# Kernel optimization log

Hardware: AMD Instinct MI355X
Metric: run time of the kernel (lower is better)

Reference implementation:

```python
import jax, jax.numpy as jnp
from jax import lax
import numpy as np

B, T, C = 32, 1024, 512
K = 3
MAX_DUR = 4            # durations drawn from [0,5) -> max value 4
L_MAX = T * MAX_DUR    # static padded mel length (torch pads to batch max; we pad to static max)
EPS = 1e-5


def conv_ln_block(x, w, b, g, beta):
    # x: [B,T,C]; torch ConvLNBlock: permute -> Conv1d(SAME) -> relu -> permute -> LayerNorm -> dropout(eval=id)
    y = lax.conv_general_dilated(x.transpose(0, 2, 1), w, (1,), 'SAME',
                                 dimension_numbers=('NCH', 'OIH', 'NCH')) + b[None, :, None]
    y = jax.nn.relu(y).transpose(0, 2, 1)  # [B,T,Cout]
    mu = y.mean(-1, keepdims=True)
    var = y.var(-1, keepdims=True)
    return (y - mu) * lax.rsqrt(var + EPS) * g + beta


def regulate(batch, durations, token_lengths):
    # Vectorized equivalent of DurationRegulator.inflate: repeat token t durations[b,t] times,
    # concatenate, pad. Implemented as cumsum + searchsorted gather (single pass, no ragged loops).
    pos = jnp.arange(T)
    valid = pos[None, :] < token_lengths[:, None]          # [B,T]
    d = jnp.where(valid, durations, 0)
    total = d.sum(axis=1)
    # torch: if durs.sum()==0 -> fill with 1
    d = jnp.where((total == 0)[:, None], valid.astype(d.dtype), d)
    total = d.sum(axis=1)                                   # [B]
    cum = jnp.cumsum(d, axis=1)                             # inclusive cumsum [B,T]
    frames = jnp.arange(L_MAX)
    idx = jax.vmap(lambda c: jnp.searchsorted(c, frames, side='right'))(cum)  # [B,L_MAX]
    idx = jnp.clip(idx, 0, T - 1)
    out = jnp.take_along_axis(batch, idx[:, :, None], axis=1)                 # [B,L_MAX,C]
    frame_mask = frames[None, :] < total[:, None]
    out = out * frame_mask[:, :, None].astype(batch.dtype)
    return out, total.astype(jnp.float32)


def setup_inputs() -> dict:
    key = jax.random.key(0)
    ks = jax.random.split(key, 8)
    batch = jax.random.normal(ks[0], (B, T, C), dtype=jnp.float32)
    token_lengths = jax.random.randint(ks[1], (B,), T // 2, T + 1).astype(jnp.int32)
    mask = jnp.arange(T)[None, :] < token_lengths[:, None]
    label_durations = jax.random.randint(ks[2], (B, T), 0, MAX_DUR + 1).astype(jnp.int32)
    s1 = 1.0 / np.sqrt(C * K)
    s2 = 1.0 / np.sqrt(C * K)
    params = {
        'conv1_w': jax.random.uniform(ks[3], (C, C, K), minval=-s1, maxval=s1, dtype=jnp.float32),
        'conv1_b': jnp.zeros((C,), jnp.float32),
        'ln1_g': jnp.ones((C,), jnp.float32), 'ln1_b': jnp.zeros((C,), jnp.float32),
        'conv2_w': jax.random.uniform(ks[4], (C, C, K), minval=-s2, maxval=s2, dtype=jnp.float32),
        'conv2_b': jnp.zeros((C,), jnp.float32),
        'ln2_g': jnp.ones((C,), jnp.float32), 'ln2_b': jnp.zeros((C,), jnp.float32),
        'lin_w': jax.random.uniform(ks[5], (C, 1), minval=-1/np.sqrt(C), maxval=1/np.sqrt(C), dtype=jnp.float32),
        'lin_b': jnp.zeros((1,), jnp.float32),
    }
    return dict(batch=batch, token_lengths=token_lengths, mask=mask,
                label_durations=label_durations, **params)


def reference(batch, token_lengths, mask, label_durations,
              conv1_w, conv1_b, ln1_g, ln1_b,
              conv2_w, conv2_b, ln2_g, ln2_b,
              lin_w, lin_b):
    # VariancePredictor: two ConvLN blocks + Linear(out_channels, 1), masked fill 0
    h = conv_ln_block(batch, conv1_w, conv1_b, ln1_g, ln1_b)
    h = conv_ln_block(h, conv2_w, conv2_b, ln2_g, ln2_b)
    predicted_durations = h @ lin_w + lin_b                      # [B,T,1]
    predicted_durations = jnp.where(mask[:, :, None], predicted_durations, 0.0)
    # label_durations provided -> regulator uses labels (training path), alpha=1
    padded_batch, mel_lengths = regulate(batch, label_durations, token_lengths)
    return padded_batch, mel_lengths, predicted_durations
```

## Files before the change

### kernel.cpp

```cpp
#include <hip/hip_runtime.h>
#include <hip/hip_bf16.h>
#include <stdint.h>


typedef _Float16 f16;
typedef _Float16 f16x8 __attribute__((ext_vector_type(8)));
typedef float f32x4 __attribute__((ext_vector_type(4)));

#define B_    32
#define T_    1024
#define TP_   1026
#define C_    512
#define LMAX_ 4096
#define KDIM  1536
#define NK    48

#define XPAD_OFF   0u
#define H1PAD_OFF  33619968u
#define W1T_OFF    67239936u
#define W2T_OFF    68812800u
#define TOT_OFF    137494528u
#define IDX_OFF    137495040u

#define AS1C(p) ((const __attribute__((address_space(1))) void*)(p))
#define AS3(p)  ((__attribute__((address_space(3))) void*)(p))

__global__ __launch_bounds__(256) void prep_pad(const float* __restrict__ batch,
                                                f16* __restrict__ xpad,
                                                f16* __restrict__ h1pad) {
    int row = blockIdx.x * 4 + (threadIdx.x >> 6);
    int lane = threadIdx.x & 63;
    int b = row / TP_, tt = row % TP_;
    size_t dsto = (size_t)row * C_ + lane * 8;
    if (tt == 0 || tt == TP_ - 1) {
        f16x8 z = {};
        *(f16x8*)(xpad + dsto) = z;
        *(f16x8*)(h1pad + dsto) = z;
    } else {
        const float* src = batch + ((size_t)(b * T_ + tt - 1)) * C_ + lane * 8;
        float4 v0 = ((const float4*)src)[0];
        float4 v1 = ((const float4*)src)[1];
        f16x8 h;
        h[0] = (f16)v0.x; h[1] = (f16)v0.y; h[2] = (f16)v0.z; h[3] = (f16)v0.w;
        h[4] = (f16)v1.x; h[5] = (f16)v1.y; h[6] = (f16)v1.z; h[7] = (f16)v1.w;
        *(f16x8*)(xpad + dsto) = h;
    }
}

__global__ __launch_bounds__(256) void prep_w(const float* __restrict__ w1,
                                              const float* __restrict__ w2,
                                              f16* __restrict__ w1t,
                                              f16* __restrict__ w2t) {
    int o = blockIdx.x;
    const float* w = blockIdx.y ? w2 : w1;
    f16* wt = blockIdx.y ? w2t : w1t;
    for (int j = threadIdx.x; j < KDIM; j += 256) {
        int tap = j >> 9, i = j & 511;
        wt[(size_t)o * KDIM + j] = (f16)w[(size_t)o * KDIM + i * 3 + tap];
    }
}

__global__ __launch_bounds__(1024) void scan_kernel(const int* __restrict__ dur,
                                                    const int* __restrict__ tlen,
                                                    int* __restrict__ idxarr,
                                                    int* __restrict__ total,
                                                    float* __restrict__ mel_out) {
    int b = blockIdx.x, t = threadIdx.x;
    __shared__ int sd[1024];
    __shared__ int sv[1024];
    int L = tlen[b];
    int valid = (t < L) ? 1 : 0;
    int d = valid ? dur[b * T_ + t] : 0;
    sd[t] = d; sv[t] = valid;
    __syncthreads();
    for (int off = 1; off < 1024; off <<= 1) {
        int x = 0, y = 0;
        if (t >= off) { x = sd[t - off]; y = sv[t - off]; }
        __syncthreads();
        sd[t] += x; sv[t] += y;
        __syncthreads();
    }
    int totd = sd[1023];
    int cur  = (totd == 0) ? sv[t] : sd[t];
    int prev = (t == 0) ? 0 : ((totd == 0) ? sv[t - 1] : sd[t - 1]);
    for (int f = prev; f < cur; f++) idxarr[b * LMAX_ + f] = t;
    if (t == 1023) {
        int tt = (totd == 0) ? sv[1023] : totd;
        total[b] = tt;
        mel_out[b] = (float)tt;
    }
}

template<int EPI>
__global__ __launch_bounds__(512, 2) void gemm_fused(const f16* __restrict__ A,
                                                     const f16* __restrict__ Bw,
                                                     const float* __restrict__ bias,
                                                     const float* __restrict__ g,
                                                     const float* __restrict__ be,
                                                     const float* __restrict__ lw,
                                                     const float* __restrict__ lb,
                                                     const int* __restrict__ tlen,
                                                     f16* __restrict__ hpad,
                                                     float* __restrict__ pred) {
    __shared__ f16 lds_[40960];
    f16* const A0 = lds_;
    f16* const A1 = lds_ + 4096;
    f16* const B0 = lds_ + 8192;
    f16* const B1 = lds_ + 24576;
    float* red = (float*)lds_;

    const int tid = threadIdx.x;
    const int lane = tid & 63;
    const int w = tid >> 6;
    const int wm = (w & 1) * 64;
    const int wn = (w >> 1) * 128;
    const int m0 = blockIdx.x * 128;
    const int arow0 = (m0 >> 10) * TP_ + (m0 & 1023);

    f32x4 acc[4][8];
#pragma unroll
    for (int i = 0; i < 4; i++)
#pragma unroll
        for (int j = 0; j < 8; j++) acc[i][j] = (f32x4){0.f, 0.f, 0.f, 0.f};

    const int perm = (lane & 3) ^ ((lane >> 2) & 3) ^ ((lane >> 4) & 3);
    const f16* aB = A + (size_t)(arow0 + w * 16 + (lane >> 2)) * C_ + perm * 8;
    const f16* bB = Bw + (size_t)(w * 16 + (lane >> 2)) * KDIM + perm * 8;

#define STAGE(Ad, Bd, kofs) do {                                              \
        __builtin_amdgcn_global_load_lds(AS1C(aB + (kofs)),                   \
                                         AS3((Ad) + w * 512), 16, 0, 0);      \
        _Pragma("unroll")                                                     \
        for (int j_ = 0; j_ < 4; j_++) {                                      \
            __builtin_amdgcn_global_load_lds(                                 \
                AS1C(bB + (size_t)(128 * j_) * KDIM + (kofs)),                \
                AS3((Bd) + (w + 8 * j_) * 512), 16, 0, 0);                    \
        }                                                                     \
    } while (0)

    STAGE(A0, B0, 0);
    __syncthreads();

    f16 *Ac = A0, *An = A1, *Bc = B0, *Bn = B1;
    for (int t = 0; t < NK; ++t) {
        if (t + 1 < NK) STAGE(An, Bn, (t + 1) * 32);
        const int base = perm * 8;
        f16x8 af[4], bf[8];
#pragma unroll
        for (int mi = 0; mi < 4; mi++)
            af[mi] = *(const f16x8*)&Ac[(wm + mi * 16 + (lane & 15)) * 32 + base];
#pragma unroll
        for (int ni = 0; ni < 8; ni++)
            bf[ni] = *(const f16x8*)&Bc[(wn + ni * 16 + (lane & 15)) * 32 + base];
#pragma unroll
        for (int mi = 0; mi < 4; mi++)
#pragma unroll
            for (int ni = 0; ni < 8; ni++)
                acc[mi][ni] = __builtin_amdgcn_mfma_f32_16x16x32_f16(
                    af[mi], bf[ni], acc[mi][ni], 0, 0, 0);
        __syncthreads();
        f16* tp;
        tp = Ac; Ac = An; An = tp;
        tp = Bc; Bc = Bn; Bn = tp;
    }
#undef STAGE

    const int col = lane & 15;
    const int row4 = (lane >> 4) * 4;
    const int nw = w >> 1;

    float bn[8];
#pragma unroll
    for (int ni = 0; ni < 8; ni++) bn[ni] = bias[wn + ni * 16 + col];
    float s_[4][4], q_[4][4];
#pragma unroll
    for (int mi = 0; mi < 4; mi++)
#pragma unroll
        for (int r = 0; r < 4; r++) { s_[mi][r] = 0.f; q_[mi][r] = 0.f; }
#pragma unroll
    for (int mi = 0; mi < 4; mi++)
#pragma unroll
        for (int ni = 0; ni < 8; ni++)
#pragma unroll
            for (int r = 0; r < 4; r++) {
                float v = acc[mi][ni][r] + bn[ni];
                v = v > 0.f ? v : 0.f;
                acc[mi][ni][r] = v;
                s_[mi][r] += v;
                q_[mi][r] += v * v;
            }
#pragma unroll
    for (int m = 8; m; m >>= 1)
#pragma unroll
        for (int mi = 0; mi < 4; mi++)
#pragma unroll
            for (int r = 0; r < 4; r++) {
                s_[mi][r] += __shfl_xor(s_[mi][r], m, 64);
                q_[mi][r] += __shfl_xor(q_[mi][r], m, 64);
            }
    if (col == 0) {
#pragma unroll
        for (int mi = 0; mi < 4; mi++)
#pragma unroll
            for (int r = 0; r < 4; r++) {
                int row = wm + mi * 16 + row4 + r;
                red[(nw * 128 + row) * 2]     = s_[mi][r];
                red[(nw * 128 + row) * 2 + 1] = q_[mi][r];
            }
    }
    __syncthreads();
    float mu_[4][4], rs_[4][4];
#pragma unroll
    for (int mi = 0; mi < 4; mi++)
#pragma unroll
        for (int r = 0; r < 4; r++) {
            int row = wm + mi * 16 + row4 + r;
            float S = red[row * 2]             + red[(128 + row) * 2]
                    + red[(256 + row) * 2]     + red[(384 + row) * 2];
            float Q = red[row * 2 + 1]         + red[(128 + row) * 2 + 1]
                    + red[(256 + row) * 2 + 1] + red[(384 + row) * 2 + 1];
            float mu = S * (1.f / 512.f);
            float x = Q * (1.f / 512.f) - mu * mu + 1e-5f;
            float rs = rsqrtf(x);
            rs = rs * (1.5f - 0.5f * x * rs * rs);
            mu_[mi][r] = mu; rs_[mi][r] = rs;
        }

    if (EPI == 0) {
        const int bb = m0 >> 10, t0 = m0 & 1023;
        f16* hbase = hpad + ((size_t)(bb * TP_ + t0 + 1)) * C_;
#pragma unroll
        for (int ni = 0; ni < 8; ni++) {
            int n = wn + ni * 16 + col;
            float gv = g[n], ev = be[n];
#pragma unroll
            for (int mi = 0; mi < 4; mi++)
#pragma unroll
                for (int r = 0; r < 4; r++) {
                    int lm = wm + mi * 16 + row4 + r;
                    float v = (acc[mi][ni][r] - mu_[mi][r]) * rs_[mi][r] * gv + ev;
                    hbase[(size_t)lm * C_ + n] = (f16)v;
                }
        }
    } else {
        float p_[4][4];
#pragma unroll
        for (int mi = 0; mi < 4; mi++)
#pragma unroll
            for (int r = 0; r < 4; r++) p_[mi][r] = 0.f;
#pragma unroll
        for (int ni = 0; ni < 8; ni++) {
            int n = wn + ni * 16 + col;
            float gv = g[n], ev = be[n], wv = lw[n];
#pragma unroll
            for (int mi = 0; mi < 4; mi++)
#pragma unroll
                for (int r = 0; r < 4; r++)
                    p_[mi][r] += ((acc[mi][ni][r] - mu_[mi][r]) * rs_[mi][r] * gv + ev) * wv;
        }
#pragma unroll
        for (int m = 8; m; m >>= 1)
#pragma unroll
            for (int mi = 0; mi < 4; mi++)
#pragma unroll
                for (int r = 0; r < 4; r++)
                    p_[mi][r] += __shfl_xor(p_[mi][r], m, 64);
        __syncthreads();
        if (col == 0) {
#pragma unroll
            for (int mi = 0; mi < 4; mi++)
#pragma unroll
                for (int r = 0; r < 4; r++)
                    red[nw * 128 + wm + mi * 16 + row4 + r] = p_[mi][r];
        }
        __syncthreads();
        if (tid < 128) {
            int m = m0 + tid;
            float p = red[tid] + red[128 + tid] + red[256 + tid] + red[384 + tid];
            int bb = m >> 10, t = m & 1023;
            pred[m] = (t < tlen[bb]) ? (p + lb[0]) : 0.f;
        }
    }
}

__global__ __launch_bounds__(256) void gather_kernel(const float* __restrict__ batch,
                                                     const int* __restrict__ idxarr,
                                                     const int* __restrict__ total,
                                                     float* __restrict__ out) {
    int gw = blockIdx.x * 4 + (threadIdx.x >> 6);
    int lane = threadIdx.x & 63;
    int b = gw >> 12;
    int l = gw & (LMAX_ - 1);
    int tot = total[b];
    float4* dst = (float4*)(out + ((size_t)b * LMAX_ + l) * C_);
    if (l < tot) {
        int idx = idxarr[gw];
        const float4* src = (const float4*)(batch + ((size_t)b * T_ + idx) * C_);
        dst[lane] = src[lane];
        dst[lane + 64] = src[lane + 64];
    } else {
        float4 z = {0.f, 0.f, 0.f, 0.f};
        dst[lane] = z;
        dst[lane + 64] = z;
    }
}

extern "C" void kernel_launch(void* const* d_in, const int* in_sizes, int n_in,
                              void* d_out, int out_size, void* d_ws, size_t ws_size,
                              hipStream_t stream) {
    const float* batch = (const float*)d_in[0];
    const int* tlen    = (const int*)d_in[1];
    const int* durs    = (const int*)d_in[3];
    const float* w1  = (const float*)d_in[4];
    const float* b1  = (const float*)d_in[5];
    const float* g1  = (const float*)d_in[6];
    const float* be1 = (const float*)d_in[7];
    const float* w2  = (const float*)d_in[8];
    const float* b2  = (const float*)d_in[9];
    const float* g2  = (const float*)d_in[10];
    const float* be2 = (const float*)d_in[11];
    const float* lw  = (const float*)d_in[12];
    const float* lb  = (const float*)d_in[13];

    float* out      = (float*)d_out;
    float* mel_out  = out + (size_t)B_ * LMAX_ * C_;
    float* pred_out = mel_out + B_;

    char* ws    = (char*)d_ws;
    f16* xpad   = (f16*)(ws + XPAD_OFF);
    f16* h1pad  = (f16*)(ws + H1PAD_OFF);
    f16* w1t    = (f16*)(ws + W1T_OFF);
    f16* w2t    = (f16*)(ws + W2T_OFF);
    int* tot    = (int*)(ws + TOT_OFF);
    int* idxarr = (int*)(ws + IDX_OFF);

    prep_pad<<<B_ * TP_ / 4, 256, 0, stream>>>(batch, xpad, h1pad);
    prep_w<<<dim3(512, 2), 256, 0, stream>>>(w1, w2, w1t, w2t);
    scan_kernel<<<B_, 1024, 0, stream>>>(durs, tlen, idxarr, tot, mel_out);
    gemm_fused<0><<<256, 512, 0, stream>>>(xpad, w1t, b1, g1, be1,
                                           nullptr, nullptr, nullptr, h1pad, nullptr);
    gemm_fused<1><<<256, 512, 0, stream>>>(h1pad, w2t, b2, g2, be2,
                                           lw, lb, tlen, nullptr, pred_out);
    gather_kernel<<<B_ * LMAX_ / 4, 256, 0, stream>>>(batch, idxarr, tot, out);
}
```

Before: 503.3 us.

## Triple-buffer GEMM LDS stages with explicit vmcnt waits and barriers

```diff
diff --git a/kernel.cpp b/kernel.cpp
--- a/kernel.cpp
+++ b/kernel.cpp
@@ -102,11 +102,13 @@
                                                      const int* __restrict__ tlen,
                                                      f16* __restrict__ hpad,
                                                      float* __restrict__ pred) {
-    __shared__ f16 lds_[40960];
+    __shared__ f16 lds_[61440];
     f16* const A0 = lds_;
     f16* const A1 = lds_ + 4096;
-    f16* const B0 = lds_ + 8192;
-    f16* const B1 = lds_ + 24576;
+    f16* const A2 = lds_ + 8192;
+    f16* const B0 = lds_ + 12288;
+    f16* const B1 = lds_ + 28672;
+    f16* const B2 = lds_ + 45056;
     float* red = (float*)lds_;
 
     const int tid = threadIdx.x;
@@ -124,6 +126,7 @@
         for (int j = 0; j < 8; j++) acc[i][j] = (f32x4){0.f, 0.f, 0.f, 0.f};
 
     const int perm = (lane & 3) ^ ((lane >> 2) & 3) ^ ((lane >> 4) & 3);
+    const int base = perm * 8;
     const f16* aB = A + (size_t)(arow0 + w * 16 + (lane >> 2)) * C_ + perm * 8;
     const f16* bB = Bw + (size_t)(w * 16 + (lane >> 2)) * KDIM + perm * 8;
 
@@ -138,31 +141,46 @@
         }                                                                     \
     } while (0)
 
+#define COMPUTE(Ac, Bc) do {                                                  \
+        f16x8 af[4], bf[8];                                                   \
+        _Pragma("unroll")                                                     \
+        for (int mi = 0; mi < 4; mi++)                                        \
+            af[mi] = *(const f16x8*)&(Ac)[(wm + mi * 16 + (lane & 15)) * 32 + base]; \
+        _Pragma("unroll")                                                     \
+        for (int ni = 0; ni < 8; ni++)                                        \
+            bf[ni] = *(const f16x8*)&(Bc)[(wn + ni * 16 + (lane & 15)) * 32 + base]; \
+        _Pragma("unroll")                                                     \
+        for (int mi = 0; mi < 4; mi++)                                        \
+            _Pragma("unroll")                                                 \
+            for (int ni = 0; ni < 8; ni++)                                    \
+                acc[mi][ni] = __builtin_amdgcn_mfma_f32_16x16x32_f16(         \
+                    af[mi], bf[ni], acc[mi][ni], 0, 0, 0);                    \
+    } while (0)
+
+#define ITER(Ac, Bc, tval, DO_STAGE, An2, Bn2, VMSTR) do {                    \
+        if (DO_STAGE) STAGE(An2, Bn2, ((tval) + 2) * 32);                     \
+        asm volatile("s_waitcnt " VMSTR ::: "memory");                        \
+        __builtin_amdgcn_s_barrier();                                         \
+        __builtin_amdgcn_sched_barrier(0);                                    \
+        COMPUTE(Ac, Bc);                                                      \
+        __builtin_amdgcn_sched_barrier(0);                                    \
+        __builtin_amdgcn_s_barrier();                                         \
+    } while (0)
+
     STAGE(A0, B0, 0);
-    __syncthreads();
-
-    f16 *Ac = A0, *An = A1, *Bc = B0, *Bn = B1;
-    for (int t = 0; t < NK; ++t) {
-        if (t + 1 < NK) STAGE(An, Bn, (t + 1) * 32);
-        const int base = perm * 8;
-        f16x8 af[4], bf[8];
-#pragma unroll
-        for (int mi = 0; mi < 4; mi++)
-            af[mi] = *(const f16x8*)&Ac[(wm + mi * 16 + (lane & 15)) * 32 + base];
-#pragma unroll
-        for (int ni = 0; ni < 8; ni++)
-            bf[ni] = *(const f16x8*)&Bc[(wn + ni * 16 + (lane & 15)) * 32 + base];
-#pragma unroll
-        for (int mi = 0; mi < 4; mi++)
-#pragma unroll
-            for (int ni = 0; ni < 8; ni++)
-                acc[mi][ni] = __builtin_amdgcn_mfma_f32_16x16x32_f16(
-                    af[mi], bf[ni], acc[mi][ni], 0, 0, 0);
-        __syncthreads();
-        f16* tp;
-        tp = Ac; Ac = An; An = tp;
-        tp = Bc; Bc = Bn; Bn = tp;
-    }
+    STAGE(A1, B1, 32);
+
+    for (int tt = 0; tt < NK - 3; tt += 3) {
+        ITER(A0, B0, tt,     1, A2, B2, "vmcnt(10)");
+        ITER(A1, B1, tt + 1, 1, A0, B0, "vmcnt(10)");
+        ITER(A2, B2, tt + 2, 1, A1, B1, "vmcnt(10)");
+    }
+    ITER(A0, B0, NK - 3, 1, A2, B2, "vmcnt(10)");
+    ITER(A1, B1, NK - 2, 0, A0, B0, "vmcnt(5)");
+    ITER(A2, B2, NK - 1, 0, A1, B1, "vmcnt(0)");
+
+#undef ITER
+#undef COMPUTE
 #undef STAGE
 
     const int col = lane & 15;
```

New measurement: 499.6 us. Within noise of the previous version (-0.7%).
